# Kernel optimization log

Hardware: AMD Instinct MI355X
Metric: run time of the kernel (lower is better)

## Reference

```python
import jax, jax.numpy as jnp
import numpy as np

N, IN_DIM, D, H, L, E, MAX_DEG = 50000, 128, 128, 16, 3, 800000, 512
C = D // H  # head dim


def _ln(x, scale, bias, eps=1e-5):
    mu = x.mean(-1, keepdims=True)
    var = ((x - mu) ** 2).mean(-1, keepdims=True)
    return (x - mu) * jax.lax.rsqrt(var + eps) * scale + bias


def setup_inputs() -> dict:
    key = jax.random.key(0)
    ks = jax.random.split(key, 20)
    s = 0.02
    inp = {
        "x": jax.random.normal(ks[0], (N, IN_DIM), jnp.float32),
        "edge_index": jax.random.randint(ks[1], (2, E), 0, N, jnp.int32),
        "W_in": jax.random.normal(ks[2], (IN_DIM, D), jnp.float32) * s,
        "b_in": jnp.zeros((D,), jnp.float32),
        "in_emb": jax.random.normal(ks[3], (MAX_DEG + 1, D), jnp.float32) * s,
        "out_emb": jax.random.normal(ks[4], (MAX_DEG + 1, D), jnp.float32) * s,
        "ln_scale": jnp.ones((L, D), jnp.float32),
        "ln_bias": jnp.zeros((L, D), jnp.float32),
        "Wq": jax.random.normal(ks[5], (L, D, D), jnp.float32) * s,
        "bq": jnp.zeros((L, D), jnp.float32),
        "Wk": jax.random.normal(ks[6], (L, D, D), jnp.float32) * s,
        "bk": jnp.zeros((L, D), jnp.float32),
        "Wv": jax.random.normal(ks[7], (L, D, D), jnp.float32) * s,
        "bv": jnp.zeros((L, D), jnp.float32),
        "Wskip": jax.random.normal(ks[8], (L, D, D), jnp.float32) * s,
        "bskip": jnp.zeros((L, D), jnp.float32),
        "Wbeta": jax.random.normal(ks[9], (L, 3 * D, 1), jnp.float32) * s,
        "fn_scale": jnp.ones((D,), jnp.float32),
        "fn_bias": jnp.zeros((D,), jnp.float32),
    }
    return inp


def _transformer_conv(h, src, tgt, Wq, bq, Wk, bk, Wv, bv, Wskip, bskip, Wbeta):
    # PyG TransformerConv, beta=True, concat=True, eval mode (no dropout)
    q = (h @ Wq + bq).reshape(N, H, C)
    k = (h @ Wk + bk).reshape(N, H, C)
    v = (h @ Wv + bv).reshape(N, H, C)
    # per-edge attention logits [E, H]
    alpha = (q[tgt] * k[src]).sum(-1) / jnp.sqrt(jnp.float32(C))
    # scatter-softmax over incoming edges of each target node
    m = jax.ops.segment_max(alpha, tgt, num_segments=N)
    ex = jnp.exp(alpha - m[tgt])
    den = jax.ops.segment_sum(ex, tgt, num_segments=N)
    w = ex / den[tgt]  # [E, H]
    msg = v[src] * w[:, :, None]  # [E, H, C]
    out = jax.ops.segment_sum(msg, tgt, num_segments=N).reshape(N, D)
    # root skip + gated beta combination
    xr = h @ Wskip + bskip
    beta = jax.nn.sigmoid(jnp.concatenate([out, xr, out - xr], axis=-1) @ Wbeta)
    return beta * xr + (1.0 - beta) * out


def reference(x, edge_index, W_in, b_in, in_emb, out_emb, ln_scale, ln_bias,
              Wq, bq, Wk, bk, Wv, bv, Wskip, bskip, Wbeta, fn_scale, fn_bias):
    src, tgt = edge_index[0], edge_index[1]
    h = x @ W_in + b_in
    # centrality encoding: in/out degree embeddings
    ones = jnp.ones((E,), jnp.float32)
    idg = jnp.clip(jax.ops.segment_sum(ones, tgt, num_segments=N), 0, MAX_DEG).astype(jnp.int32)
    odg = jnp.clip(jax.ops.segment_sum(ones, src, num_segments=N), 0, MAX_DEG).astype(jnp.int32)
    h = h + in_emb[idg] + out_emb[odg]
    for l in range(L):
        hn = _ln(h, ln_scale[l], ln_bias[l])
        h = h + _transformer_conv(hn, src, tgt, Wq[l], bq[l], Wk[l], bk[l],
                                  Wv[l], bv[l], Wskip[l], bskip[l], Wbeta[l])
    return _ln(h, fn_scale, fn_bias)
```

## Files before the change

### kernel.cpp

```cpp
#include <hip/hip_runtime.h>
#include <math.h>
#include <stdint.h>

#define NN 50000
#define DM 128
#define NH 16
#define HC 8
#define NL 3
#define NE 800000
#define MAXDEG 512
#define NRG 1563

#define NB2 782
#define NBLK 256
#define CNTN (NB2 * NBLK)
#define SC1 196
#define RNG 4
#define REP 16

typedef __attribute__((ext_vector_type(8))) short short8;
typedef __attribute__((ext_vector_type(4))) float f32x4;
typedef __attribute__((ext_vector_type(2))) float f32x2;

static __device__ __forceinline__ unsigned short f2bf(float x) {
    union { float f; unsigned int u; } v; v.f = x;
    unsigned int r = (v.u + 0x7fffu + ((v.u >> 16) & 1u)) >> 16;
    return (unsigned short)r;
}
static __device__ __forceinline__ float bf2f(unsigned short b) {
    union { unsigned int u; float f; } v; v.u = ((unsigned int)b) << 16;
    return v.f;
}

__global__ __launch_bounds__(1024) void hist_out_kernel(const int* __restrict__ ei,
                                                        unsigned int* __restrict__ part) {
    __shared__ unsigned int hp[8192];
    int rg = blockIdx.x;
    int rp = blockIdx.y;
    int t = threadIdx.x;
    for (int i = t; i < 8192; i += 1024) hp[i] = 0;
    __syncthreads();
    int lo = rg << 14;
    for (int e = rp * 1024 + t; e < NE; e += REP * 1024) {
        int s = ei[e] - lo;
        if ((unsigned)s < 16384u)
            atomicAdd(&hp[s >> 1], (s & 1) ? 0x10000u : 1u);
    }
    __syncthreads();
    unsigned int* pp = part + (size_t)(rg * REP + rp) * 8192;
    for (int i = t; i < 8192; i += 1024) pp[i] = hp[i];
}
__global__ __launch_bounds__(256) void hist_reduce_kernel(const unsigned int* __restrict__ part,
                                                          int* __restrict__ outdeg) {
    int wd = blockIdx.x * 256 + threadIdx.x;
    if (wd >= 25000) return;
    int rg = wd >> 13, lw = wd & 8191;
    unsigned int sum = 0;
#pragma unroll
    for (int r = 0; r < REP; r++)
        sum += part[(size_t)(rg * REP + r) * 8192 + lw];
    outdeg[2 * wd] = sum & 0xffff;
    if (2 * wd + 1 < NN) outdeg[2 * wd + 1] = sum >> 16;
}

__global__ __launch_bounds__(256) void p1_count_kernel(const int* __restrict__ ei,
                                                       int* __restrict__ cnt) {
    __shared__ int hh[NB2];
    int t = threadIdx.x, blk = blockIdx.x;
    for (int b = t; b < NB2; b += 256) hh[b] = 0;
    __syncthreads();
    for (int e = blk * 256 + t; e < NE; e += NBLK * 256)
        atomicAdd(&hh[ei[NE + e] >> 6], 1);
    __syncthreads();
    for (int b = t; b < NB2; b += 256) cnt[b * NBLK + blk] = hh[b];
}

__global__ __launch_bounds__(1024) void gscan1_kernel(int* __restrict__ data,
                                                      int* __restrict__ bsum, int n) {
    __shared__ int sd[1024];
    int t = threadIdx.x;
    int i = blockIdx.x * 1024 + t;
    int val = (i < n) ? data[i] : 0;
    sd[t] = val;
    __syncthreads();
    for (int d = 1; d < 1024; d <<= 1) {
        int x = (t >= d) ? sd[t - d] : 0;
        __syncthreads();
        sd[t] += x;
        __syncthreads();
    }
    if (i < n) data[i] = sd[t] - val;
    if (t == 1023) bsum[blockIdx.x] = sd[1023];
}
__global__ void gscan2_kernel(const int* __restrict__ bsum, int* __restrict__ bpre, int nb) {
    int run = 0;
    for (int i = 0; i < nb; i++) { bpre[i] = run; run += bsum[i]; }
}
__global__ __launch_bounds__(1024) void gscan3_kernel(int* __restrict__ data,
                                                      const int* __restrict__ bpre, int n) {
    int i = blockIdx.x * 1024 + threadIdx.x;
    if (i < n) data[i] += bpre[blockIdx.x];
}

__global__ __launch_bounds__(256) void p3_scatter_kernel(const int* __restrict__ ei,
                                                         const int* __restrict__ cnt,
                                                         int* __restrict__ tmp) {
    __shared__ int hh[NB2];
    int t = threadIdx.x, blk = blockIdx.x;
    for (int b = t; b < NB2; b += 256) hh[b] = cnt[b * NBLK + blk];
    __syncthreads();
    for (int e = blk * 256 + t; e < NE; e += NBLK * 256) {
        int s = ei[e], tg = ei[NE + e];
        int pos = atomicAdd(&hh[tg >> 6], 1);
        tmp[pos] = ((tg & 63) << 16) | s;
    }
}

__global__ __launch_bounds__(256) void p4_fine_kernel(const int* __restrict__ tmp,
                                                      const int* __restrict__ cnt,
                                                      int* __restrict__ off,
                                                      int* __restrict__ indeg,
                                                      int* __restrict__ srcs) {
    __shared__ int c64[64], x64[64], cur[64];
    int b = blockIdx.x, t = threadIdx.x;
    int e0 = cnt[b * NBLK];
    int e1 = (b == NB2 - 1) ? NE : cnt[(b + 1) * NBLK];
    if (t < 64) c64[t] = 0;
    __syncthreads();
    for (int i = e0 + t; i < e1; i += 256) atomicAdd(&c64[(tmp[i] >> 16) & 63], 1);
    __syncthreads();
    if (t == 0) {
        int run = 0;
        for (int j = 0; j < 64; j++) { x64[j] = run; cur[j] = e0 + run; run += c64[j]; }
    }
    __syncthreads();
    if (t < 64) {
        int node = b * 64 + t;
        if (node <= NN) off[node] = e0 + x64[t];
        if (node < NN) indeg[node] = c64[t];
    }
    __syncthreads();
    for (int i = e0 + t; i < e1; i += 256) {
        int w = tmp[i];
        int pos = atomicAdd(&cur[(w >> 16) & 63], 1);
        srcs[pos] = w & 0xffff;
    }
}

__global__ __launch_bounds__(256) void wprep_kernel(const float* __restrict__ Wq,
                                                    const float* __restrict__ Wk,
                                                    const float* __restrict__ Wv,
                                                    const float* __restrict__ Ws,
                                                    const float* __restrict__ Win,
                                                    unsigned short* __restrict__ Wt) {
    __shared__ unsigned short lds[128 * 130];
    int bid = blockIdx.x;
    const float* W;
    if (bid == 12) {
        W = Win;
    } else {
        int l = bid >> 2, m = bid & 3;
        W = (m == 0 ? Wq : m == 1 ? Wk : m == 2 ? Wv : Ws) + (size_t)l * DM * DM;
    }
    unsigned short* out = Wt + (size_t)bid * DM * DM;
    int t = threadIdx.x;
    for (int i = t; i < DM * DM; i += 256) {
        int kk = i >> 7, c = i & 127;
        lds[kk * 130 + c] = f2bf(W[i]);
    }
    __syncthreads();
    for (int o = t; o < DM * DM; o += 256) {
        int c = o >> 7, kk = o & 127;
        out[o] = lds[kk * 130 + c];
    }
}

__global__ __launch_bounds__(256) void xcast_kernel(const float* __restrict__ x,
                                                    unsigned short* __restrict__ xb) {
    int i = blockIdx.x * 256 + threadIdx.x;
    float4 xv = ((const float4*)x)[i];
    ushort4 o;
    o.x = f2bf(xv.x); o.y = f2bf(xv.y); o.z = f2bf(xv.z); o.w = f2bf(xv.w);
    ((ushort4*)xb)[i] = o;
}

__global__ __launch_bounds__(256) void gemm_in_mfma(const unsigned short* __restrict__ xb,
                                                    const unsigned short* __restrict__ Wt,
                                                    const float* __restrict__ b,
                                                    const float* __restrict__ in_emb,
                                                    const float* __restrict__ out_emb,
                                                    const int* __restrict__ indeg,
                                                    const int* __restrict__ outdeg,
                                                    float* __restrict__ h) {
    int w = threadIdx.x >> 6;
    int l = threadIdx.x & 63;
    int lr = l & 15, lc = l >> 4;
    int colbase = (w & 1) * 64;
    int rhalf = w >> 1;

    short8 bfrag[4][4];
#pragma unroll
    for (int ct = 0; ct < 4; ct++) {
        const unsigned short* bp = Wt + (size_t)(colbase + ct * 16 + lr) * DM;
#pragma unroll
        for (int kk = 0; kk < 4; kk++)
            bfrag[ct][kk] = *(const short8*)(bp + kk * 32 + lc * 8);
    }

    for (int rg = blockIdx.x * 2 + rhalf; rg < NRG; rg += gridDim.x * 2) {
        int n0 = rg * 32;
        short8 afrag[2][4];
#pragma unroll
        for (int rt = 0; rt < 2; rt++) {
            int row = n0 + rt * 16 + lr;
            if (row >= NN) row = NN - 1;
            const unsigned short* ap = xb + (size_t)row * DM;
#pragma unroll
            for (int kk = 0; kk < 4; kk++)
                afrag[rt][kk] = *(const short8*)(ap + kk * 32 + lc * 8);
        }
        f32x4 acc[4][2];
#pragma unroll
        for (int ct = 0; ct < 4; ct++)
#pragma unroll
            for (int nt = 0; nt < 2; nt++)
                acc[ct][nt] = (f32x4){0.f, 0.f, 0.f, 0.f};
#pragma unroll
        for (int kk = 0; kk < 4; kk++)
#pragma unroll
            for (int ct = 0; ct < 4; ct++)
#pragma unroll
                for (int nt = 0; nt < 2; nt++)
                    acc[ct][nt] = __builtin_amdgcn_mfma_f32_16x16x32_bf16(
                        bfrag[ct][kk], afrag[nt][kk], acc[ct][nt], 0, 0, 0);
#pragma unroll
        for (int nt = 0; nt < 2; nt++) {
            int node = n0 + nt * 16 + lr;
            if (node < NN) {
                int id = min(indeg[node], MAXDEG);
                int od = min(outdeg[node], MAXDEG);
#pragma unroll
                for (int ct = 0; ct < 4; ct++) {
                    int ch = colbase + ct * 16 + lc * 4;
                    float4 bb = *(const float4*)(b + ch);
                    float4 ie = *(const float4*)(in_emb + (size_t)id * DM + ch);
                    float4 oe = *(const float4*)(out_emb + (size_t)od * DM + ch);
                    float4 o;
                    o.x = acc[ct][nt][0] + bb.x + ie.x + oe.x;
                    o.y = acc[ct][nt][1] + bb.y + ie.y + oe.y;
                    o.z = acc[ct][nt][2] + bb.z + ie.z + oe.z;
                    o.w = acc[ct][nt][3] + bb.w + ie.w + oe.w;
                    *(float4*)(h + (size_t)node * DM + ch) = o;
                }
            }
        }
    }
}

static __device__ __forceinline__ void ln_body(const float* __restrict__ hp,
                                               const float* __restrict__ sc,
                                               const float* __restrict__ bi,
                                               int lane, float* o0, float* o1) {
    float v0 = hp[lane], v1 = hp[lane + 64];
    float s = v0 + v1;
#pragma unroll
    for (int d = 32; d; d >>= 1) s += __shfl_xor(s, d);
    float mu = s * (1.f / 128.f);
    float d0 = v0 - mu, d1 = v1 - mu;
    float vs = d0 * d0 + d1 * d1;
#pragma unroll
    for (int d = 32; d; d >>= 1) vs += __shfl_xor(vs, d);
    float rstd = rsqrtf(vs * (1.f / 128.f) + 1e-5f);
    *o0 = d0 * rstd * sc[lane] + bi[lane];
    *o1 = d1 * rstd * sc[lane + 64] + bi[lane + 64];
}

__global__ __launch_bounds__(256) void ln_bf16_kernel(const float* __restrict__ h,
                                                      const float* __restrict__ sc,
                                                      const float* __restrict__ bi,
                                                      unsigned short* __restrict__ o) {
    int row = blockIdx.x * 4 + (threadIdx.x >> 6);
    int lane = threadIdx.x & 63;
    float a, b;
    ln_body(h + (size_t)row * DM, sc, bi, lane, &a, &b);
    unsigned short* op = o + (size_t)row * DM;
    op[lane] = f2bf(a);
    op[lane + 64] = f2bf(b);
}

__global__ __launch_bounds__(256) void ln_f32_kernel(const float* __restrict__ h,
                                                     const float* __restrict__ sc,
                                                     const float* __restrict__ bi,
                                                     float* __restrict__ o) {
    int row = blockIdx.x * 4 + (threadIdx.x >> 6);
    int lane = threadIdx.x & 63;
    float a, b;
    ln_body(h + (size_t)row * DM, sc, bi, lane, &a, &b);
    float* op = o + (size_t)row * DM;
    op[lane] = a;
    op[lane + 64] = b;
}

__global__ __launch_bounds__(512) void gemm_qkvs_mfma(const unsigned short* __restrict__ hn,
                                                      const unsigned short* __restrict__ Wt,
                                                      const float* __restrict__ bq, const float* __restrict__ bk,
                                                      const float* __restrict__ bv, const float* __restrict__ bs,
                                                      unsigned short* __restrict__ q,
                                                      unsigned char* __restrict__ kv8,
                                                      unsigned short* __restrict__ xrb) {
    int w = threadIdx.x >> 6;
    int l = threadIdx.x & 63;
    int lr = l & 15, lc = l >> 4;
    int colbase = w * 64;
    int m = w >> 1;
    int cmbase = (w & 1) * 64;

    const float* bptr = (m == 0 ? bq : m == 1 ? bk : m == 2 ? bv : bs);
    short8 bfrag[4][4];
    float biasv[4][4];
#pragma unroll
    for (int ct = 0; ct < 4; ct++) {
        int col = colbase + ct * 16 + lr;
        const unsigned short* bp = Wt + (size_t)col * DM;
#pragma unroll
        for (int kk = 0; kk < 4; kk++)
            bfrag[ct][kk] = *(const short8*)(bp + kk * 32 + lc * 8);
#pragma unroll
        for (int j = 0; j < 4; j++)
            biasv[ct][j] = bptr[cmbase + ct * 16 + lc * 4 + j];
    }

    for (int rg = blockIdx.x; rg < NRG; rg += gridDim.x) {
        int n0 = rg * 32;
        short8 afrag[2][4];
#pragma unroll
        for (int nt = 0; nt < 2; nt++) {
            int row = n0 + nt * 16 + lr;
            if (row >= NN) row = NN - 1;
            const unsigned short* ap = hn + (size_t)row * DM;
#pragma unroll
            for (int kk = 0; kk < 4; kk++)
                afrag[nt][kk] = *(const short8*)(ap + kk * 32 + lc * 8);
        }
        f32x4 acc[4][2];
#pragma unroll
        for (int ct = 0; ct < 4; ct++)
#pragma unroll
            for (int nt = 0; nt < 2; nt++)
                acc[ct][nt] = (f32x4){0.f, 0.f, 0.f, 0.f};
#pragma unroll
        for (int kk = 0; kk < 4; kk++)
#pragma unroll
            for (int ct = 0; ct < 4; ct++)
#pragma unroll
                for (int nt = 0; nt < 2; nt++)
                    acc[ct][nt] = __builtin_amdgcn_mfma_f32_16x16x32_bf16(
                        bfrag[ct][kk], afrag[nt][kk], acc[ct][nt], 0, 0, 0);

        if (m == 0 || m == 3) {
            unsigned short* dst = (m == 0) ? q : xrb;
#pragma unroll
            for (int nt = 0; nt < 2; nt++) {
                int node = n0 + nt * 16 + lr;
                if (node < NN) {
#pragma unroll
                    for (int ct = 0; ct < 4; ct++) {
                        int ch = cmbase + ct * 16 + lc * 4;
                        ushort4 st;
                        st.x = f2bf(acc[ct][nt][0] + biasv[ct][0]);
                        st.y = f2bf(acc[ct][nt][1] + biasv[ct][1]);
                        st.z = f2bf(acc[ct][nt][2] + biasv[ct][2]);
                        st.w = f2bf(acc[ct][nt][3] + biasv[ct][3]);
                        *(ushort4*)(dst + (size_t)node * DM + ch) = st;
                    }
                }
            }
        } else {
            unsigned char* base = kv8 + ((m == 1) ? 0 : 4);
#pragma unroll
            for (int nt = 0; nt < 2; nt++) {
                int node = n0 + nt * 16 + lr;
                if (node < NN) {
#pragma unroll
                    for (int ct = 0; ct < 4; ct++) {
                        int ch = cmbase + ct * 16 + lc * 4;
                        int wd = __builtin_amdgcn_cvt_pk_fp8_f32(
                            acc[ct][nt][0] + biasv[ct][0],
                            acc[ct][nt][1] + biasv[ct][1], 0, false);
                        wd = __builtin_amdgcn_cvt_pk_fp8_f32(
                            acc[ct][nt][2] + biasv[ct][2],
                            acc[ct][nt][3] + biasv[ct][3], wd, true);
                        *(unsigned int*)(base + (size_t)node * 256 + (ch >> 2) * 8) =
                            (unsigned int)wd;
                    }
                }
            }
        }
    }
}

__global__ __launch_bounds__(256) void attn_fused_kernel(const int* __restrict__ off,
                                                         const int* __restrict__ srcs,
                                                         const unsigned short* __restrict__ q,
                                                         const unsigned char* __restrict__ kv8,
                                                         const unsigned short* __restrict__ xrb,
                                                         const float* __restrict__ Wb,
                                                         float* __restrict__ h,
                                                         const float* __restrict__ nsc,
                                                         const float* __restrict__ nbi,
                                                         unsigned short* __restrict__ hn_out) {
    int wv = threadIdx.x >> 6;
    int L = threadIdx.x & 63;
    int half = L >> 5, L5 = L & 31;
    int n = blockIdx.x * 4 + wv;
    int o0 = off[n], o1 = off[n + 1];
    int c4 = L5 * 4;
    const float isq = 0.35355339059f;

    ushort4 qu = *(const ushort4*)(q + (size_t)n * DM + c4);
    float q0 = bf2f(qu.x) * isq, q1 = bf2f(qu.y) * isq,
          q2 = bf2f(qu.z) * isq, q3 = bf2f(qu.w) * isq;

    float den = 0.f, a0 = 0.f, a1 = 0.f, a2 = 0.f, a3 = 0.f;
    int p = o0;
    for (; p + 16 <= o1; p += 16) {
        int sj[8];
#pragma unroll
        for (int j = 0; j < 8; j++) sj[j] = srcs[p + 2 * j + half];
        uint2 uu[8];
#pragma unroll
        for (int j = 0; j < 8; j++)
            uu[j] = *(const uint2*)(kv8 + (size_t)sj[j] * 256 + L5 * 8);
#pragma unroll
        for (int j = 0; j < 8; j++) {
            f32x2 k01 = __builtin_amdgcn_cvt_pk_f32_fp8(uu[j].x, false);
            f32x2 k23 = __builtin_amdgcn_cvt_pk_f32_fp8(uu[j].x, true);
            f32x2 v01 = __builtin_amdgcn_cvt_pk_f32_fp8(uu[j].y, false);
            f32x2 v23 = __builtin_amdgcn_cvt_pk_f32_fp8(uu[j].y, true);
            float d = q0 * k01.x + q1 * k01.y + q2 * k23.x + q3 * k23.y;
            d += __shfl_xor(d, 1);
            float e2 = __expf(d);
            den += e2;
            a0 += e2 * v01.x;
            a1 += e2 * v01.y;
            a2 += e2 * v23.x;
            a3 += e2 * v23.y;
        }
    }
    if (p < o1) {
        int sj[8];
#pragma unroll
        for (int j = 0; j < 8; j++) {
            int e = p + 2 * j + half;
            sj[j] = (e < o1) ? srcs[e] : 0;
        }
        uint2 uu[8];
#pragma unroll
        for (int j = 0; j < 8; j++)
            uu[j] = *(const uint2*)(kv8 + (size_t)sj[j] * 256 + L5 * 8);
#pragma unroll
        for (int j = 0; j < 8; j++) {
            int e = p + 2 * j + half;
            f32x2 k01 = __builtin_amdgcn_cvt_pk_f32_fp8(uu[j].x, false);
            f32x2 k23 = __builtin_amdgcn_cvt_pk_f32_fp8(uu[j].x, true);
            f32x2 v01 = __builtin_amdgcn_cvt_pk_f32_fp8(uu[j].y, false);
            f32x2 v23 = __builtin_amdgcn_cvt_pk_f32_fp8(uu[j].y, true);
            float d = q0 * k01.x + q1 * k01.y + q2 * k23.x + q3 * k23.y;
            d += __shfl_xor(d, 1);
            float e2 = (e < o1) ? __expf(d) : 0.f;
            den += e2;
            a0 += e2 * v01.x;
            a1 += e2 * v01.y;
            a2 += e2 * v23.x;
            a3 += e2 * v23.y;
        }
    }
    den += __shfl_xor(den, 32);
    a0 += __shfl_xor(a0, 32);
    a1 += __shfl_xor(a1, 32);
    a2 += __shfl_xor(a2, 32);
    a3 += __shfl_xor(a3, 32);

    float inv = (den > 0.f) ? 1.f / den : 0.f;
    float o0v = a0 * inv, o1v = a1 * inv, o2v = a2 * inv, o3v = a3 * inv;

    ushort4 xu = *(const ushort4*)(xrb + (size_t)n * DM + c4);
    float x0 = bf2f(xu.x), x1 = bf2f(xu.y), x2 = bf2f(xu.z), x3 = bf2f(xu.w);
    float c = o0v * Wb[c4] + o1v * Wb[c4 + 1] + o2v * Wb[c4 + 2] + o3v * Wb[c4 + 3]
            + x0 * Wb[DM + c4] + x1 * Wb[DM + c4 + 1]
            + x2 * Wb[DM + c4 + 2] + x3 * Wb[DM + c4 + 3]
            + (o0v - x0) * Wb[2 * DM + c4] + (o1v - x1) * Wb[2 * DM + c4 + 1]
            + (o2v - x2) * Wb[2 * DM + c4 + 2] + (o3v - x3) * Wb[2 * DM + c4 + 3];
    if (half) c = 0.f;
#pragma unroll
    for (int d2 = 32; d2; d2 >>= 1) c += __shfl_xor(c, d2);
    float beta = 1.f / (1.f + __expf(-c));

    size_t idx = (size_t)n * DM + c4;
    float4 hv = *(const float4*)(h + idx);
    hv.x += beta * x0 + (1.f - beta) * o0v;
    hv.y += beta * x1 + (1.f - beta) * o1v;
    hv.z += beta * x2 + (1.f - beta) * o2v;
    hv.w += beta * x3 + (1.f - beta) * o3v;
    if (half == 0) *(float4*)(h + idx) = hv;

    if (hn_out) {
        float s = hv.x + hv.y + hv.z + hv.w;
#pragma unroll
        for (int d2 = 16; d2; d2 >>= 1) s += __shfl_xor(s, d2);
        float mu = s * (1.f / 128.f);
        float d0 = hv.x - mu, d1 = hv.y - mu, d2_ = hv.z - mu, d3 = hv.w - mu;
        float vs = d0 * d0 + d1 * d1 + d2_ * d2_ + d3 * d3;
#pragma unroll
        for (int d2 = 16; d2; d2 >>= 1) vs += __shfl_xor(vs, d2);
        float rstd = rsqrtf(vs * (1.f / 128.f) + 1e-5f);
        float4 scv = *(const float4*)(nsc + c4);
        float4 biv = *(const float4*)(nbi + c4);
        ushort4 o;
        o.x = f2bf(d0 * rstd * scv.x + biv.x);
        o.y = f2bf(d1 * rstd * scv.y + biv.y);
        o.z = f2bf(d2_ * rstd * scv.z + biv.z);
        o.w = f2bf(d3 * rstd * scv.w + biv.w);
        if (half == 0) *(ushort4*)(hn_out + idx) = o;
    }
}

static inline char* alignup(char* p) {
    return (char*)(((uintptr_t)p + 255) & ~(uintptr_t)255);
}

extern "C" void kernel_launch(void* const* d_in, const int* in_sizes, int n_in,
                              void* d_out, int out_size, void* d_ws, size_t ws_size,
                              hipStream_t stream) {
    const float* x       = (const float*)d_in[0];
    const int*   ei      = (const int*)d_in[1];
    const float* W_in    = (const float*)d_in[2];
    const float* b_in    = (const float*)d_in[3];
    const float* in_emb  = (const float*)d_in[4];
    const float* out_emb = (const float*)d_in[5];
    const float* ln_sc   = (const float*)d_in[6];
    const float* ln_bi   = (const float*)d_in[7];
    const float* Wq      = (const float*)d_in[8];
    const float* bq      = (const float*)d_in[9];
    const float* Wk      = (const float*)d_in[10];
    const float* bk      = (const float*)d_in[11];
    const float* Wv      = (const float*)d_in[12];
    const float* bv      = (const float*)d_in[13];
    const float* Wsk     = (const float*)d_in[14];
    const float* bsk     = (const float*)d_in[15];
    const float* Wbeta   = (const float*)d_in[16];
    const float* fn_sc   = (const float*)d_in[17];
    const float* fn_bi   = (const float*)d_in[18];

    char* w = (char*)d_ws;
    int* indeg  = (int*)w; w = alignup(w + (size_t)NN * 4);
    int* outdeg = (int*)w; w = alignup(w + (size_t)NN * 4);
    int* off    = (int*)w; w = alignup(w + (size_t)(NN + 1) * 4);
    int* srcs   = (int*)w; w = alignup(w + (size_t)NE * 4);
    int* tmp    = (int*)w; w = alignup(w + (size_t)NE * 4);
    int* cnt    = (int*)w; w = alignup(w + (size_t)CNTN * 4);
    int* bsum   = (int*)w; w = alignup(w + (size_t)SC1 * 4);
    int* bpre   = (int*)w; w = alignup(w + (size_t)SC1 * 4);
    unsigned int* hpart = (unsigned int*)w; w = alignup(w + (size_t)RNG * REP * 8192 * 4);
    float* h    = (float*)w; w = alignup(w + (size_t)NN * DM * 4);
    unsigned short* hn  = (unsigned short*)w; w = alignup(w + (size_t)NN * DM * 2);
    unsigned short* q   = (unsigned short*)w; w = alignup(w + (size_t)NN * DM * 2);
    unsigned short* xrb = (unsigned short*)w; w = alignup(w + (size_t)NN * DM * 2);
    unsigned char*  kv8 = (unsigned char*)w;  w = alignup(w + (size_t)NN * 256);
    unsigned short* xb  = (unsigned short*)w; w = alignup(w + (size_t)NN * DM * 2);
    unsigned short* Wt  = (unsigned short*)w; w = alignup(w + (size_t)13 * DM * DM * 2);

    hist_out_kernel<<<dim3(RNG, REP), 1024, 0, stream>>>(ei, hpart);
    hist_reduce_kernel<<<98, 256, 0, stream>>>(hpart, outdeg);
    p1_count_kernel<<<NBLK, 256, 0, stream>>>(ei, cnt);
    gscan1_kernel<<<SC1, 1024, 0, stream>>>(cnt, bsum, CNTN);
    gscan2_kernel<<<1, 1, 0, stream>>>(bsum, bpre, SC1);
    gscan3_kernel<<<SC1, 1024, 0, stream>>>(cnt, bpre, CNTN);
    p3_scatter_kernel<<<NBLK, 256, 0, stream>>>(ei, cnt, tmp);
    p4_fine_kernel<<<NB2, 256, 0, stream>>>(tmp, cnt, off, indeg, srcs);

    wprep_kernel<<<13, 256, 0, stream>>>(Wq, Wk, Wv, Wsk, W_in, Wt);
    xcast_kernel<<<NN * DM / 4 / 256, 256, 0, stream>>>(x, xb);

    gemm_in_mfma<<<391, 256, 0, stream>>>(xb, Wt + (size_t)12 * DM * DM, b_in,
                                          in_emb, out_emb, indeg, outdeg, h);
    ln_bf16_kernel<<<NN / 4, 256, 0, stream>>>(h, ln_sc, ln_bi, hn);
    for (int l = 0; l < NL; l++) {
        gemm_qkvs_mfma<<<391, 512, 0, stream>>>(hn,
            Wt + (size_t)l * 4 * DM * DM,
            bq + l * DM, bk + l * DM, bv + l * DM, bsk + l * DM,
            q, kv8, xrb);
        bool last = (l == NL - 1);
        attn_fused_kernel<<<NN / 4, 256, 0, stream>>>(off, srcs, q, kv8, xrb,
            Wbeta + (size_t)l * 3 * DM, h,
            last ? (const float*)nullptr : ln_sc + (l + 1) * DM,
            last ? (const float*)nullptr : ln_bi + (l + 1) * DM,
            last ? (unsigned short*)nullptr : hn);
    }
    ln_f32_kernel<<<NN / 4, 256, 0, stream>>>(h, fn_sc, fn_bi, (float*)d_out);
}
```

Baseline: 360.2 us.

## Interleave fp8 K/V per head and fuse final layernorm into last attention

The fp8 K/V buffer is rearranged so each head's 8 K bytes and 8 V bytes sit together in 16 bytes. The attention kernel now assigns one lane per head with four edge groups per wave, loading a uint4 per edge. This removes the cross-lane shuffle in the dot product and halves the number of gather instructions. The final layernorm is fused into the last layer's attention kernel, which drops a separate kernel and one extra read and write of h, at the cost of more registers per lane for the 8-wide accumulators.

```diff
diff --git a/kernel.cpp b/kernel.cpp
--- a/kernel.cpp
+++ b/kernel.cpp
@@ -288,19 +288,6 @@
     op[lane + 64] = f2bf(b);
 }
 
-__global__ __launch_bounds__(256) void ln_f32_kernel(const float* __restrict__ h,
-                                                     const float* __restrict__ sc,
-                                                     const float* __restrict__ bi,
-                                                     float* __restrict__ o) {
-    int row = blockIdx.x * 4 + (threadIdx.x >> 6);
-    int lane = threadIdx.x & 63;
-    float a, b;
-    ln_body(h + (size_t)row * DM, sc, bi, lane, &a, &b);
-    float* op = o + (size_t)row * DM;
-    op[lane] = a;
-    op[lane + 64] = b;
-}
-
 __global__ __launch_bounds__(512) void gemm_qkvs_mfma(const unsigned short* __restrict__ hn,
                                                       const unsigned short* __restrict__ Wt,
                                                       const float* __restrict__ bq, const float* __restrict__ bk,
@@ -376,7 +363,7 @@
                 }
             }
         } else {
-            unsigned char* base = kv8 + ((m == 1) ? 0 : 4);
+            int mofs = (m == 1) ? 0 : 8;
 #pragma unroll
             for (int nt = 0; nt < 2; nt++) {
                 int node = n0 + nt * 16 + lr;
@@ -390,7 +377,8 @@
                         wd = __builtin_amdgcn_cvt_pk_fp8_f32(
                             acc[ct][nt][2] + biasv[ct][2],
                             acc[ct][nt][3] + biasv[ct][3], wd, true);
-                        *(unsigned int*)(base + (size_t)node * 256 + (ch >> 2) * 8) =
+                        int off2 = (ch >> 3) * 16 + mofs + (ch & 4);
+                        *(unsigned int*)(kv8 + (size_t)node * 256 + off2) =
                             (unsigned int)wd;
                     }
                 }
@@ -408,120 +396,190 @@
                                                          float* __restrict__ h,
                                                          const float* __restrict__ nsc,
                                                          const float* __restrict__ nbi,
-                                                         unsigned short* __restrict__ hn_out) {
+                                                         unsigned short* __restrict__ hn_out,
+                                                         const float* __restrict__ fsc,
+                                                         const float* __restrict__ fbi,
+                                                         float* __restrict__ fout) {
     int wv = threadIdx.x >> 6;
     int L = threadIdx.x & 63;
-    int half = L >> 5, L5 = L & 31;
+    int eg = L >> 4;
+    int hh = L & 15;
     int n = blockIdx.x * 4 + wv;
     int o0 = off[n], o1 = off[n + 1];
-    int c4 = L5 * 4;
+    int ch0 = hh * 8;
     const float isq = 0.35355339059f;
 
-    ushort4 qu = *(const ushort4*)(q + (size_t)n * DM + c4);
-    float q0 = bf2f(qu.x) * isq, q1 = bf2f(qu.y) * isq,
-          q2 = bf2f(qu.z) * isq, q3 = bf2f(qu.w) * isq;
-
-    float den = 0.f, a0 = 0.f, a1 = 0.f, a2 = 0.f, a3 = 0.f;
+    short8 qv = *(const short8*)(q + (size_t)n * DM + ch0);
+    float qf[8];
+#pragma unroll
+    for (int c = 0; c < 8; c++) qf[c] = bf2f((unsigned short)qv[c]) * isq;
+
+    float den = 0.f, a[8];
+#pragma unroll
+    for (int c = 0; c < 8; c++) a[c] = 0.f;
+
     int p = o0;
     for (; p + 16 <= o1; p += 16) {
-        int sj[8];
-#pragma unroll
-        for (int j = 0; j < 8; j++) sj[j] = srcs[p + 2 * j + half];
-        uint2 uu[8];
-#pragma unroll
-        for (int j = 0; j < 8; j++)
-            uu[j] = *(const uint2*)(kv8 + (size_t)sj[j] * 256 + L5 * 8);
-#pragma unroll
-        for (int j = 0; j < 8; j++) {
-            f32x2 k01 = __builtin_amdgcn_cvt_pk_f32_fp8(uu[j].x, false);
-            f32x2 k23 = __builtin_amdgcn_cvt_pk_f32_fp8(uu[j].x, true);
-            f32x2 v01 = __builtin_amdgcn_cvt_pk_f32_fp8(uu[j].y, false);
-            f32x2 v23 = __builtin_amdgcn_cvt_pk_f32_fp8(uu[j].y, true);
-            float d = q0 * k01.x + q1 * k01.y + q2 * k23.x + q3 * k23.y;
-            d += __shfl_xor(d, 1);
+        int sj[4];
+#pragma unroll
+        for (int r = 0; r < 4; r++) sj[r] = srcs[p + r * 4 + eg];
+        uint4 uu[4];
+#pragma unroll
+        for (int r = 0; r < 4; r++)
+            uu[r] = *(const uint4*)(kv8 + (size_t)sj[r] * 256 + hh * 16);
+#pragma unroll
+        for (int r = 0; r < 4; r++) {
+            f32x2 k01 = __builtin_amdgcn_cvt_pk_f32_fp8(uu[r].x, false);
+            f32x2 k23 = __builtin_amdgcn_cvt_pk_f32_fp8(uu[r].x, true);
+            f32x2 k45 = __builtin_amdgcn_cvt_pk_f32_fp8(uu[r].y, false);
+            f32x2 k67 = __builtin_amdgcn_cvt_pk_f32_fp8(uu[r].y, true);
+            float d = qf[0] * k01.x + qf[1] * k01.y + qf[2] * k23.x + qf[3] * k23.y
+                    + qf[4] * k45.x + qf[5] * k45.y + qf[6] * k67.x + qf[7] * k67.y;
             float e2 = __expf(d);
+            f32x2 v01 = __builtin_amdgcn_cvt_pk_f32_fp8(uu[r].z, false);
+            f32x2 v23 = __builtin_amdgcn_cvt_pk_f32_fp8(uu[r].z, true);
+            f32x2 v45 = __builtin_amdgcn_cvt_pk_f32_fp8(uu[r].w, false);
+            f32x2 v67 = __builtin_amdgcn_cvt_pk_f32_fp8(uu[r].w, true);
             den += e2;
-            a0 += e2 * v01.x;
-            a1 += e2 * v01.y;
-            a2 += e2 * v23.x;
-            a3 += e2 * v23.y;
+            a[0] += e2 * v01.x; a[1] += e2 * v01.y;
+            a[2] += e2 * v23.x; a[3] += e2 * v23.y;
+            a[4] += e2 * v45.x; a[5] += e2 * v45.y;
+            a[6] += e2 * v67.x; a[7] += e2 * v67.y;
         }
     }
     if (p < o1) {
-        int sj[8];
-#pragma unroll
-        for (int j = 0; j < 8; j++) {
-            int e = p + 2 * j + half;
-            sj[j] = (e < o1) ? srcs[e] : 0;
-        }
-        uint2 uu[8];
-#pragma unroll
-        for (int j = 0; j < 8; j++)
-            uu[j] = *(const uint2*)(kv8 + (size_t)sj[j] * 256 + L5 * 8);
-#pragma unroll
-        for (int j = 0; j < 8; j++) {
-            int e = p + 2 * j + half;
-            f32x2 k01 = __builtin_amdgcn_cvt_pk_f32_fp8(uu[j].x, false);
-            f32x2 k23 = __builtin_amdgcn_cvt_pk_f32_fp8(uu[j].x, true);
-            f32x2 v01 = __builtin_amdgcn_cvt_pk_f32_fp8(uu[j].y, false);
-            f32x2 v23 = __builtin_amdgcn_cvt_pk_f32_fp8(uu[j].y, true);
-            float d = q0 * k01.x + q1 * k01.y + q2 * k23.x + q3 * k23.y;
-            d += __shfl_xor(d, 1);
+        int sj[4];
+#pragma unroll
+        for (int r = 0; r < 4; r++) {
+            int e = p + r * 4 + eg;
+            sj[r] = (e < o1) ? srcs[e] : 0;
+        }
+        uint4 uu[4];
+#pragma unroll
+        for (int r = 0; r < 4; r++)
+            uu[r] = *(const uint4*)(kv8 + (size_t)sj[r] * 256 + hh * 16);
+#pragma unroll
+        for (int r = 0; r < 4; r++) {
+            int e = p + r * 4 + eg;
+            f32x2 k01 = __builtin_amdgcn_cvt_pk_f32_fp8(uu[r].x, false);
+            f32x2 k23 = __builtin_amdgcn_cvt_pk_f32_fp8(uu[r].x, true);
+            f32x2 k45 = __builtin_amdgcn_cvt_pk_f32_fp8(uu[r].y, false);
+            f32x2 k67 = __builtin_amdgcn_cvt_pk_f32_fp8(uu[r].y, true);
+            float d = qf[0] * k01.x + qf[1] * k01.y + qf[2] * k23.x + qf[3] * k23.y
+                    + qf[4] * k45.x + qf[5] * k45.y + qf[6] * k67.x + qf[7] * k67.y;
             float e2 = (e < o1) ? __expf(d) : 0.f;
+            f32x2 v01 = __builtin_amdgcn_cvt_pk_f32_fp8(uu[r].z, false);
+            f32x2 v23 = __builtin_amdgcn_cvt_pk_f32_fp8(uu[r].z, true);
+            f32x2 v45 = __builtin_amdgcn_cvt_pk_f32_fp8(uu[r].w, false);
+            f32x2 v67 = __builtin_amdgcn_cvt_pk_f32_fp8(uu[r].w, true);
             den += e2;
-            a0 += e2 * v01.x;
-            a1 += e2 * v01.y;
-            a2 += e2 * v23.x;
-            a3 += e2 * v23.y;
-        }
-    }
-    den += __shfl_xor(den, 32);
-    a0 += __shfl_xor(a0, 32);
-    a1 += __shfl_xor(a1, 32);
-    a2 += __shfl_xor(a2, 32);
-    a3 += __shfl_xor(a3, 32);
+            a[0] += e2 * v01.x; a[1] += e2 * v01.y;
+            a[2] += e2 * v23.x; a[3] += e2 * v23.y;
+            a[4] += e2 * v45.x; a[5] += e2 * v45.y;
+            a[6] += e2 * v67.x; a[7] += e2 * v67.y;
+        }
+    }
+    den += __shfl_xor(den, 16); den += __shfl_xor(den, 32);
+#pragma unroll
+    for (int c = 0; c < 8; c++) {
+        a[c] += __shfl_xor(a[c], 16);
+        a[c] += __shfl_xor(a[c], 32);
+    }
 
     float inv = (den > 0.f) ? 1.f / den : 0.f;
-    float o0v = a0 * inv, o1v = a1 * inv, o2v = a2 * inv, o3v = a3 * inv;
-
-    ushort4 xu = *(const ushort4*)(xrb + (size_t)n * DM + c4);
-    float x0 = bf2f(xu.x), x1 = bf2f(xu.y), x2 = bf2f(xu.z), x3 = bf2f(xu.w);
-    float c = o0v * Wb[c4] + o1v * Wb[c4 + 1] + o2v * Wb[c4 + 2] + o3v * Wb[c4 + 3]
-            + x0 * Wb[DM + c4] + x1 * Wb[DM + c4 + 1]
-            + x2 * Wb[DM + c4 + 2] + x3 * Wb[DM + c4 + 3]
-            + (o0v - x0) * Wb[2 * DM + c4] + (o1v - x1) * Wb[2 * DM + c4 + 1]
-            + (o2v - x2) * Wb[2 * DM + c4 + 2] + (o3v - x3) * Wb[2 * DM + c4 + 3];
-    if (half) c = 0.f;
-#pragma unroll
-    for (int d2 = 32; d2; d2 >>= 1) c += __shfl_xor(c, d2);
-    float beta = 1.f / (1.f + __expf(-c));
-
-    size_t idx = (size_t)n * DM + c4;
-    float4 hv = *(const float4*)(h + idx);
-    hv.x += beta * x0 + (1.f - beta) * o0v;
-    hv.y += beta * x1 + (1.f - beta) * o1v;
-    hv.z += beta * x2 + (1.f - beta) * o2v;
-    hv.w += beta * x3 + (1.f - beta) * o3v;
-    if (half == 0) *(float4*)(h + idx) = hv;
-
-    if (hn_out) {
-        float s = hv.x + hv.y + hv.z + hv.w;
-#pragma unroll
-        for (int d2 = 16; d2; d2 >>= 1) s += __shfl_xor(s, d2);
+    float ov[8];
+#pragma unroll
+    for (int c = 0; c < 8; c++) ov[c] = a[c] * inv;
+
+    short8 xv = *(const short8*)(xrb + (size_t)n * DM + ch0);
+    float xf[8];
+#pragma unroll
+    for (int c = 0; c < 8; c++) xf[c] = bf2f((unsigned short)xv[c]);
+
+    float cpar = 0.f;
+#pragma unroll
+    for (int c = 0; c < 8; c++) {
+        int ch = ch0 + c;
+        cpar += ov[c] * Wb[ch] + xf[c] * Wb[DM + ch] + (ov[c] - xf[c]) * Wb[2 * DM + ch];
+    }
+#pragma unroll
+    for (int d2 = 1; d2 <= 8; d2 <<= 1) cpar += __shfl_xor(cpar, d2);
+    float beta = 1.f / (1.f + __expf(-cpar));
+
+    size_t idx = (size_t)n * DM + ch0;
+    float4 hl0 = *(const float4*)(h + idx);
+    float4 hl1 = *(const float4*)(h + idx + 4);
+    float hv[8] = {hl0.x, hl0.y, hl0.z, hl0.w, hl1.x, hl1.y, hl1.z, hl1.w};
+#pragma unroll
+    for (int c = 0; c < 8; c++)
+        hv[c] += beta * xf[c] + (1.f - beta) * ov[c];
+
+    if (fout) {
+        float s = 0.f;
+#pragma unroll
+        for (int c = 0; c < 8; c++) s += hv[c];
+#pragma unroll
+        for (int d2 = 1; d2 <= 8; d2 <<= 1) s += __shfl_xor(s, d2);
         float mu = s * (1.f / 128.f);
-        float d0 = hv.x - mu, d1 = hv.y - mu, d2_ = hv.z - mu, d3 = hv.w - mu;
-        float vs = d0 * d0 + d1 * d1 + d2_ * d2_ + d3 * d3;
-#pragma unroll
-        for (int d2 = 16; d2; d2 >>= 1) vs += __shfl_xor(vs, d2);
+        float vs = 0.f;
+#pragma unroll
+        for (int c = 0; c < 8; c++) { float dv = hv[c] - mu; vs += dv * dv; }
+#pragma unroll
+        for (int d2 = 1; d2 <= 8; d2 <<= 1) vs += __shfl_xor(vs, d2);
         float rstd = rsqrtf(vs * (1.f / 128.f) + 1e-5f);
-        float4 scv = *(const float4*)(nsc + c4);
-        float4 biv = *(const float4*)(nbi + c4);
-        ushort4 o;
-        o.x = f2bf(d0 * rstd * scv.x + biv.x);
-        o.y = f2bf(d1 * rstd * scv.y + biv.y);
-        o.z = f2bf(d2_ * rstd * scv.z + biv.z);
-        o.w = f2bf(d3 * rstd * scv.w + biv.w);
-        if (half == 0) *(ushort4*)(hn_out + idx) = o;
+        if (eg == 0) {
+            float4 s0 = *(const float4*)(fsc + ch0);
+            float4 s1 = *(const float4*)(fsc + ch0 + 4);
+            float4 b0 = *(const float4*)(fbi + ch0);
+            float4 b1 = *(const float4*)(fbi + ch0 + 4);
+            float4 o0v, o1v;
+            o0v.x = (hv[0] - mu) * rstd * s0.x + b0.x;
+            o0v.y = (hv[1] - mu) * rstd * s0.y + b0.y;
+            o0v.z = (hv[2] - mu) * rstd * s0.z + b0.z;
+            o0v.w = (hv[3] - mu) * rstd * s0.w + b0.w;
+            o1v.x = (hv[4] - mu) * rstd * s1.x + b1.x;
+            o1v.y = (hv[5] - mu) * rstd * s1.y + b1.y;
+            o1v.z = (hv[6] - mu) * rstd * s1.z + b1.z;
+            o1v.w = (hv[7] - mu) * rstd * s1.w + b1.w;
+            *(float4*)(fout + idx) = o0v;
+            *(float4*)(fout + idx + 4) = o1v;
+        }
+    } else {
+        if (eg == 0) {
+            float4 h0 = {hv[0], hv[1], hv[2], hv[3]};
+            float4 h1 = {hv[4], hv[5], hv[6], hv[7]};
+            *(float4*)(h + idx) = h0;
+            *(float4*)(h + idx + 4) = h1;
+        }
+        float s = 0.f;
+#pragma unroll
+        for (int c = 0; c < 8; c++) s += hv[c];
+#pragma unroll
+        for (int d2 = 1; d2 <= 8; d2 <<= 1) s += __shfl_xor(s, d2);
+        float mu = s * (1.f / 128.f);
+        float vs = 0.f;
+#pragma unroll
+        for (int c = 0; c < 8; c++) { float dv = hv[c] - mu; vs += dv * dv; }
+#pragma unroll
+        for (int d2 = 1; d2 <= 8; d2 <<= 1) vs += __shfl_xor(vs, d2);
+        float rstd = rsqrtf(vs * (1.f / 128.f) + 1e-5f);
+        if (eg == 0) {
+            ushort4 w0, w1;
+            float4 s0 = *(const float4*)(nsc + ch0);
+            float4 s1 = *(const float4*)(nsc + ch0 + 4);
+            float4 b0 = *(const float4*)(nbi + ch0);
+            float4 b1 = *(const float4*)(nbi + ch0 + 4);
+            w0.x = f2bf((hv[0] - mu) * rstd * s0.x + b0.x);
+            w0.y = f2bf((hv[1] - mu) * rstd * s0.y + b0.y);
+            w0.z = f2bf((hv[2] - mu) * rstd * s0.z + b0.z);
+            w0.w = f2bf((hv[3] - mu) * rstd * s0.w + b0.w);
+            w1.x = f2bf((hv[4] - mu) * rstd * s1.x + b1.x);
+            w1.y = f2bf((hv[5] - mu) * rstd * s1.y + b1.y);
+            w1.z = f2bf((hv[6] - mu) * rstd * s1.z + b1.z);
+            w1.w = f2bf((hv[7] - mu) * rstd * s1.w + b1.w);
+            *(ushort4*)(hn_out + idx) = w0;
+            *(ushort4*)(hn_out + idx + 4) = w1;
+        }
     }
 }
 
@@ -595,7 +653,9 @@
             Wbeta + (size_t)l * 3 * DM, h,
             last ? (const float*)nullptr : ln_sc + (l + 1) * DM,
             last ? (const float*)nullptr : ln_bi + (l + 1) * DM,
-            last ? (unsigned short*)nullptr : hn);
-    }
-    ln_f32_kernel<<<NN / 4, 256, 0, stream>>>(h, fn_sc, fn_bi, (float*)d_out);
-}
+            last ? (unsigned short*)nullptr : hn,
+            last ? fn_sc : (const float*)nullptr,
+            last ? fn_bi : (const float*)nullptr,
+            last ? (float*)d_out : (float*)nullptr);
+    }
+}
```

Result: slower. 371.7 us (+3.2%).
